# Performance work log

Hardware: AMD Instinct MI355X
Metric: run time of the kernel (lower is better)

## Reference

```python
import jax, jax.numpy as jnp
import numpy as np

LEAK = 0.01  # F.leaky_relu default negative_slope


def projection(p, cam, res):
    # Weak-perspective projection to normalized [-1,1] image coords.
    # cam = [s, tx, ty]; p [B,N,3] -> [B,N,2]
    s = cam[:, 0][:, None, None]
    t = cam[:, None, 1:3]
    return s * (p[..., :2] + t)


def grid_sample_points(im_feat, pts):
    # Bilinear grid_sample with align_corners=True, zeros padding,
    # specialized to a [B,N,1,2] point grid (matches points.unsqueeze(2)).
    # im_feat [B,C,H,W], pts [B,N,2] in [-1,1] -> [B,C,N]
    B, C, H, W = im_feat.shape
    N = pts.shape[1]
    x = (pts[..., 0] + 1.0) * 0.5 * (W - 1)
    y = (pts[..., 1] + 1.0) * 0.5 * (H - 1)
    x0 = jnp.floor(x)
    y0 = jnp.floor(y)
    x1 = x0 + 1.0
    y1 = y0 + 1.0
    wx1 = x - x0
    wx0 = 1.0 - wx1
    wy1 = y - y0
    wy0 = 1.0 - wy1
    feat_flat = im_feat.reshape(B, C, H * W)

    def gather(xi, yi, w):
        valid = (xi >= 0) & (xi <= W - 1) & (yi >= 0) & (yi <= H - 1)
        xc = jnp.clip(xi, 0, W - 1).astype(jnp.int32)
        yc = jnp.clip(yi, 0, H - 1).astype(jnp.int32)
        idx = (yc * W + xc)[:, None, :]  # [B,1,N]
        g = jnp.take_along_axis(feat_flat, jnp.broadcast_to(idx, (B, C, N)), axis=2)
        return g * (w * valid.astype(w.dtype))[:, None, :]

    return (gather(x0, y0, wx0 * wy0) + gather(x1, y0, wx1 * wy0)
            + gather(x0, y1, wx0 * wy1) + gather(x1, y1, wx1 * wy1))


def reduce_dim(feat, W0, b0, W1, b1, W2, b2):
    # feat [B,C0,N]; Conv1d kernel_size=1 == channel matmul.
    def conv1x1(x, W, b):
        return jnp.einsum('oc,bcn->bon', W, x) + b[None, :, None]

    y = jax.nn.leaky_relu(conv1x1(feat, W0, b0), LEAK)
    y = jax.nn.leaky_relu(conv1x1(jnp.concatenate([y, feat], axis=1), W1, b1), LEAK)
    y = conv1x1(jnp.concatenate([y, feat], axis=1), W2, b2)
    y = jax.nn.relu(y)  # last_op
    return y.reshape(y.shape[0], -1)  # [B, C_p*N]


def setup_inputs() -> dict:
    key = jax.random.key(0)
    ks = jax.random.split(key, 9)
    B, N, C, H, Wd = 64, 431, 256, 56, 56
    dims = [256, 128, 64, 5]
    p = jax.random.normal(ks[0], (B, N, 3), jnp.float32)
    cam = jax.random.uniform(ks[1], (B, 3), jnp.float32)
    s_feat = jax.random.normal(ks[2], (B, C, H, Wd), jnp.float32)
    W0 = jax.random.normal(ks[3], (dims[1], dims[0]), jnp.float32) * 0.02
    b0 = jnp.zeros((dims[1],), jnp.float32)
    W1 = jax.random.normal(ks[4], (dims[2], dims[1] + dims[0]), jnp.float32) * 0.02
    b1 = jnp.zeros((dims[2],), jnp.float32)
    W2 = jax.random.normal(ks[5], (dims[3], dims[2] + dims[0]), jnp.float32) * 0.02
    b2 = jnp.zeros((dims[3],), jnp.float32)
    return {"p": p, "cam": cam, "s_feat": s_feat,
            "W0": W0, "b0": b0, "W1": W1, "b1": b1, "W2": W2, "b2": b2,
            "res": 224}


def reference(p, cam, s_feat, W0, b0, W1, b1, W2, b2, res):
    p2d = projection(p, cam, res)                 # [B,N,2]
    point_feat = grid_sample_points(s_feat, p2d)  # [B,C_s,N]
    return reduce_dim(point_feat, W0, b0, W1, b1, W2, b2)  # [B, C_p*N]
```

## Files before the change

kernel.cpp:

```cpp
#include <hip/hip_runtime.h>


#define B_   64
#define N_   431
#define C_   256
#define H_   56
#define W_   56
#define HW_  (H_ * W_)
#define PPB  16
#define NT_  27

#define FS   264
#define Y0S  136
#define Y1S  72

typedef __attribute__((ext_vector_type(8))) short short8;
typedef __attribute__((ext_vector_type(4))) float f32x4;

__device__ __forceinline__ ushort f2bf(float f) {
    unsigned u = __float_as_uint(f);
    u += 0x7fffu + ((u >> 16) & 1u);
    return (ushort)(u >> 16);
}
__device__ __forceinline__ float bf2f(ushort h) {
    return __uint_as_float((unsigned)h << 16);
}

__global__ void convert_weights(const float* __restrict__ W0,
                                const float* __restrict__ W1,
                                const float* __restrict__ W2,
                                ushort* __restrict__ W0b,
                                ushort* __restrict__ W1b,
                                ushort* __restrict__ W2p)
{
    const int total = 128 * 256 + 64 * 384 + 16 * 320;
    for (int i = blockIdx.x * 256 + threadIdx.x; i < total; i += gridDim.x * 256) {
        if (i < 128 * 256) {
            W0b[i] = f2bf(W0[i]);
        } else if (i < 128 * 256 + 64 * 384) {
            const int j = i - 128 * 256;
            W1b[j] = f2bf(W1[j]);
        } else {
            const int j = i - (128 * 256 + 64 * 384);
            const int r = j / 320, c = j - r * 320;
            W2p[j] = (r < 5) ? f2bf(W2[r * 320 + c]) : (ushort)0;
        }
    }
}

__global__ __launch_bounds__(256, 4) void transpose_bf16(
    const float* __restrict__ in, ushort* __restrict__ out)
{
    __shared__ float tile[64][69];
    const int pix0 = blockIdx.x * 64;
    const int c0   = blockIdx.y * 64;
    const int b    = blockIdx.z;
    const int t    = threadIdx.x;

    {
        const int cr = t >> 4;
        const int p4 = (t & 15) * 4;
        const float* inb = in + ((size_t)b * C_ + c0) * HW_ + pix0;
        #pragma unroll
        for (int i = 0; i < 4; ++i) {
            const int cc = cr + i * 16;
            const float4 v = *(const float4*)(inb + (size_t)cc * HW_ + p4);
            tile[cc][p4 + 0] = v.x;
            tile[cc][p4 + 1] = v.y;
            tile[cc][p4 + 2] = v.z;
            tile[cc][p4 + 3] = v.w;
        }
    }
    __syncthreads();
    {
        const int c4 = (t & 15) * 4;
        const int pr = t >> 4;
        ushort* outb = out + ((size_t)b * HW_ + pix0) * C_ + c0;
        #pragma unroll
        for (int i = 0; i < 4; ++i) {
            const int pp = pr + i * 16;
            ushort4 v;
            v.x = f2bf(tile[c4 + 0][pp]);
            v.y = f2bf(tile[c4 + 1][pp]);
            v.z = f2bf(tile[c4 + 2][pp]);
            v.w = f2bf(tile[c4 + 3][pp]);
            *(ushort4*)(outb + (size_t)pp * C_ + c4) = v;
        }
    }
}

__global__ __launch_bounds__(256, 4) void maf_mfma_kernel(
    const float* __restrict__ p,
    const float* __restrict__ cam,
    const ushort* __restrict__ tf,
    const ushort* __restrict__ W0b,
    const float* __restrict__ b0,
    const ushort* __restrict__ W1b,
    const float* __restrict__ b1,
    const ushort* __restrict__ W2p,
    const float* __restrict__ b2,
    float* __restrict__ out)
{
    __shared__ ushort feat_s[PPB * FS];
    __shared__ ushort y0_s[PPB * Y0S];
    __shared__ ushort y1_s[PPB * Y1S];

    const int tid = threadIdx.x;
    const int w   = tid >> 6;
    const int l   = tid & 63;
    const int m   = l & 15;
    const int q   = l >> 4;
    const int b   = blockIdx.y;
    const int n0  = blockIdx.x * PPB;

    const float s  = cam[b * 3 + 0];
    const float tx = cam[b * 3 + 1];
    const float ty = cam[b * 3 + 2];

    {
        const ushort* __restrict__ tb = tf + (size_t)b * HW_ * C_;
        const int c4 = l * 4;
        #pragma unroll
        for (int i = 0; i < 4; ++i) {
            const int pp = w * 4 + i;
            const int n  = n0 + pp;
            ushort4 r = {0, 0, 0, 0};
            if (n < N_) {
                const float px = p[((size_t)b * N_ + n) * 3 + 0];
                const float py = p[((size_t)b * N_ + n) * 3 + 1];
                const float x = (s * (px + tx) + 1.f) * 0.5f * (float)(W_ - 1);
                const float y = (s * (py + ty) + 1.f) * 0.5f * (float)(H_ - 1);
                const float x0f = floorf(x), y0f = floorf(y);
                const float wx1 = x - x0f, wx0 = 1.f - wx1;
                const float wy1 = y - y0f, wy0 = 1.f - wy1;
                const int ix0 = (int)x0f, iy0 = (int)y0f;
                const int ix1 = ix0 + 1,  iy1 = iy0 + 1;
                const bool vx0 = (ix0 >= 0) & (ix0 <= W_ - 1);
                const bool vx1 = (ix1 >= 0) & (ix1 <= W_ - 1);
                const bool vy0 = (iy0 >= 0) & (iy0 <= H_ - 1);
                const bool vy1 = (iy1 >= 0) & (iy1 <= H_ - 1);
                const int cx0 = min(max(ix0, 0), W_ - 1);
                const int cx1 = min(max(ix1, 0), W_ - 1);
                const int cy0 = min(max(iy0, 0), H_ - 1);
                const int cy1 = min(max(iy1, 0), H_ - 1);
                const float w00 = (vx0 & vy0) ? wx0 * wy0 : 0.f;
                const float w10 = (vx1 & vy0) ? wx1 * wy0 : 0.f;
                const float w01 = (vx0 & vy1) ? wx0 * wy1 : 0.f;
                const float w11 = (vx1 & vy1) ? wx1 * wy1 : 0.f;
                const ushort4 f00 = *(const ushort4*)(tb + (size_t)(cy0 * W_ + cx0) * C_ + c4);
                const ushort4 f10 = *(const ushort4*)(tb + (size_t)(cy0 * W_ + cx1) * C_ + c4);
                const ushort4 f01 = *(const ushort4*)(tb + (size_t)(cy1 * W_ + cx0) * C_ + c4);
                const ushort4 f11 = *(const ushort4*)(tb + (size_t)(cy1 * W_ + cx1) * C_ + c4);
                r.x = f2bf(w00 * bf2f(f00.x) + w10 * bf2f(f10.x) + w01 * bf2f(f01.x) + w11 * bf2f(f11.x));
                r.y = f2bf(w00 * bf2f(f00.y) + w10 * bf2f(f10.y) + w01 * bf2f(f01.y) + w11 * bf2f(f11.y));
                r.z = f2bf(w00 * bf2f(f00.z) + w10 * bf2f(f10.z) + w01 * bf2f(f01.z) + w11 * bf2f(f11.z));
                r.w = f2bf(w00 * bf2f(f00.w) + w10 * bf2f(f10.w) + w01 * bf2f(f01.w) + w11 * bf2f(f11.w));
            }
            *(ushort4*)&feat_s[pp * FS + c4] = r;
        }
    }
    __syncthreads();

    {
        f32x4 acc0 = {0.f, 0.f, 0.f, 0.f};
        f32x4 acc1 = {0.f, 0.f, 0.f, 0.f};
        const ushort* __restrict__ ar  = feat_s + m * FS + 8 * q;
        const ushort* __restrict__ wr0 = W0b + ((size_t)(2 * w) * 16 + m) * 256 + 8 * q;
        const ushort* __restrict__ wr1 = W0b + ((size_t)(2 * w + 1) * 16 + m) * 256 + 8 * q;
        #pragma unroll
        for (int ks = 0; ks < 8; ++ks) {
            const short8 a  = *(const short8*)(ar + 32 * ks);
            const short8 w0 = *(const short8*)(wr0 + 32 * ks);
            const short8 w1 = *(const short8*)(wr1 + 32 * ks);
            acc0 = __builtin_amdgcn_mfma_f32_16x16x32_bf16(a, w0, acc0, 0, 0, 0);
            acc1 = __builtin_amdgcn_mfma_f32_16x16x32_bf16(a, w1, acc1, 0, 0, 0);
        }
        const int o0 = (2 * w) * 16 + m, o1 = o0 + 16;
        const float bias0 = b0[o0], bias1 = b0[o1];
        #pragma unroll
        for (int r = 0; r < 4; ++r) {
            float v0 = acc0[r] + bias0; v0 = (v0 > 0.f) ? v0 : 0.01f * v0;
            float v1 = acc1[r] + bias1; v1 = (v1 > 0.f) ? v1 : 0.01f * v1;
            y0_s[(q * 4 + r) * Y0S + o0] = f2bf(v0);
            y0_s[(q * 4 + r) * Y0S + o1] = f2bf(v1);
        }
    }
    __syncthreads();

    {
        f32x4 acc = {0.f, 0.f, 0.f, 0.f};
        const ushort* __restrict__ wr = W1b + ((size_t)w * 16 + m) * 384 + 8 * q;
        #pragma unroll
        for (int ks = 0; ks < 12; ++ks) {
            short8 a;
            if (ks < 4) a = *(const short8*)(y0_s  + m * Y0S + 32 * ks + 8 * q);
            else        a = *(const short8*)(feat_s + m * FS + 32 * ks - 128 + 8 * q);
            const short8 bb = *(const short8*)(wr + 32 * ks);
            acc = __builtin_amdgcn_mfma_f32_16x16x32_bf16(a, bb, acc, 0, 0, 0);
        }
        const int o = w * 16 + m;
        const float bias = b1[o];
        #pragma unroll
        for (int r = 0; r < 4; ++r) {
            float v = acc[r] + bias; v = (v > 0.f) ? v : 0.01f * v;
            y1_s[(q * 4 + r) * Y1S + o] = f2bf(v);
        }
    }
    __syncthreads();

    if (w == 0) {
        f32x4 acc = {0.f, 0.f, 0.f, 0.f};
        const ushort* __restrict__ wr = W2p + (size_t)m * 320 + 8 * q;
        #pragma unroll
        for (int ks = 0; ks < 10; ++ks) {
            short8 a;
            if (ks < 2) a = *(const short8*)(y1_s + m * Y1S + 32 * ks + 8 * q);
            else        a = *(const short8*)(feat_s + m * FS + 32 * ks - 64 + 8 * q);
            const short8 bb = *(const short8*)(wr + 32 * ks);
            acc = __builtin_amdgcn_mfma_f32_16x16x32_bf16(a, bb, acc, 0, 0, 0);
        }
        if (m < 5) {
            const float bias = b2[m];
            #pragma unroll
            for (int r = 0; r < 4; ++r) {
                const int n = n0 + q * 4 + r;
                if (n < N_) {
                    float v = acc[r] + bias;
                    out[((size_t)b * 5 + m) * N_ + n] = (v > 0.f) ? v : 0.f;
                }
            }
        }
    }
}

__global__ __launch_bounds__(256, 4) void maf_fallback_kernel(
    const float* __restrict__ p, const float* __restrict__ cam,
    const float* __restrict__ sfeat,
    const float* __restrict__ W0, const float* __restrict__ b0,
    const float* __restrict__ W1, const float* __restrict__ b1,
    const float* __restrict__ W2, const float* __restrict__ b2,
    float* __restrict__ out)
{
    __shared__ float feat_s[PPB][C_ + 4];
    __shared__ float y0_s[PPB][128 + 4];
    __shared__ float y1_s[PPB][64 + 4];

    const int tid = threadIdx.x;
    const int b   = blockIdx.y;
    const int n0  = blockIdx.x * PPB;
    const float s  = cam[b * 3 + 0];
    const float tx = cam[b * 3 + 1];
    const float ty = cam[b * 3 + 2];
    {
        const int c = tid;
        const float* __restrict__ fb = sfeat + ((size_t)b * C_ + c) * HW_;
        for (int pp = 0; pp < PPB; ++pp) {
            const int n = n0 + pp;
            float val = 0.f;
            if (n < N_) {
                const float px = p[((size_t)b * N_ + n) * 3 + 0];
                const float py = p[((size_t)b * N_ + n) * 3 + 1];
                const float x = (s * (px + tx) + 1.f) * 0.5f * (float)(W_ - 1);
                const float y = (s * (py + ty) + 1.f) * 0.5f * (float)(H_ - 1);
                const float x0f = floorf(x), y0f = floorf(y);
                const float wx1 = x - x0f, wx0 = 1.f - wx1;
                const float wy1 = y - y0f, wy0 = 1.f - wy1;
                const int ix0 = (int)x0f, iy0 = (int)y0f;
                const int ix1 = ix0 + 1,  iy1 = iy0 + 1;
                const bool vx0 = (ix0 >= 0) & (ix0 <= W_ - 1);
                const bool vx1 = (ix1 >= 0) & (ix1 <= W_ - 1);
                const bool vy0 = (iy0 >= 0) & (iy0 <= H_ - 1);
                const bool vy1 = (iy1 >= 0) & (iy1 <= H_ - 1);
                const int cx0 = min(max(ix0, 0), W_ - 1);
                const int cx1 = min(max(ix1, 0), W_ - 1);
                const int cy0 = min(max(iy0, 0), H_ - 1);
                const int cy1 = min(max(iy1, 0), H_ - 1);
                const float w00 = (vx0 & vy0) ? wx0 * wy0 : 0.f;
                const float w10 = (vx1 & vy0) ? wx1 * wy0 : 0.f;
                const float w01 = (vx0 & vy1) ? wx0 * wy1 : 0.f;
                const float w11 = (vx1 & vy1) ? wx1 * wy1 : 0.f;
                val = w00 * fb[cy0 * W_ + cx0] + w10 * fb[cy0 * W_ + cx1]
                    + w01 * fb[cy1 * W_ + cx0] + w11 * fb[cy1 * W_ + cx1];
            }
            feat_s[pp][c] = val;
        }
    }
    __syncthreads();
    {
        const int o = tid & 127, pg = tid >> 7, p0 = pg * 8;
        const float* __restrict__ wr = W0 + (size_t)o * 256;
        float acc[8] = {0, 0, 0, 0, 0, 0, 0, 0};
        for (int k = 0; k < 256; k += 4) {
            const float4 w = *(const float4*)(wr + k);
            for (int i = 0; i < 8; ++i) {
                const float4 f = *(const float4*)&feat_s[p0 + i][k];
                acc[i] += w.x * f.x + w.y * f.y + w.z * f.z + w.w * f.w;
            }
        }
        const float bias = b0[o];
        for (int i = 0; i < 8; ++i) {
            const float v = acc[i] + bias;
            y0_s[p0 + i][o] = (v > 0.f) ? v : 0.01f * v;
        }
    }
    __syncthreads();
    {
        const int o = tid & 63, pg = tid >> 6, p0 = pg * 4;
        const float* __restrict__ wr = W1 + (size_t)o * 384;
        float acc[4] = {0, 0, 0, 0};
        for (int k = 0; k < 128; k += 4) {
            const float4 w = *(const float4*)(wr + k);
            for (int i = 0; i < 4; ++i) {
                const float4 f = *(const float4*)&y0_s[p0 + i][k];
                acc[i] += w.x * f.x + w.y * f.y + w.z * f.z + w.w * f.w;
            }
        }
        for (int k = 0; k < 256; k += 4) {
            const float4 w = *(const float4*)(wr + 128 + k);
            for (int i = 0; i < 4; ++i) {
                const float4 f = *(const float4*)&feat_s[p0 + i][k];
                acc[i] += w.x * f.x + w.y * f.y + w.z * f.z + w.w * f.w;
            }
        }
        const float bias = b1[o];
        for (int i = 0; i < 4; ++i) {
            const float v = acc[i] + bias;
            y1_s[p0 + i][o] = (v > 0.f) ? v : 0.01f * v;
        }
    }
    __syncthreads();
    if (tid < 80) {
        const int o = tid >> 4, pp = tid & 15;
        const float* __restrict__ wr = W2 + (size_t)o * 320;
        float acc = 0.f;
        for (int k = 0; k < 64; k += 4) {
            const float4 w = *(const float4*)(wr + k);
            const float4 f = *(const float4*)&y1_s[pp][k];
            acc += w.x * f.x + w.y * f.y + w.z * f.z + w.w * f.w;
        }
        for (int k = 0; k < 256; k += 4) {
            const float4 w = *(const float4*)(wr + 64 + k);
            const float4 f = *(const float4*)&feat_s[pp][k];
            acc += w.x * f.x + w.y * f.y + w.z * f.z + w.w * f.w;
        }
        const int n = n0 + pp;
        if (n < N_) {
            float v = acc + b2[o];
            out[((size_t)b * 5 + o) * N_ + n] = (v > 0.f) ? v : 0.f;
        }
    }
}

extern "C" void kernel_launch(void* const* d_in, const int* in_sizes, int n_in,
                              void* d_out, int out_size, void* d_ws, size_t ws_size,
                              hipStream_t stream) {
    const float* p     = (const float*)d_in[0];
    const float* cam   = (const float*)d_in[1];
    const float* sfeat = (const float*)d_in[2];
    const float* W0    = (const float*)d_in[3];
    const float* b0    = (const float*)d_in[4];
    const float* W1    = (const float*)d_in[5];
    const float* b1    = (const float*)d_in[6];
    const float* W2    = (const float*)d_in[7];
    const float* b2    = (const float*)d_in[8];
    float* out = (float*)d_out;

    const size_t tf_elems = (size_t)B_ * HW_ * C_;
    size_t off = tf_elems;
    const size_t w0_off = off; off += 128 * 256;
    const size_t w1_off = off; off += 64 * 384;
    const size_t w2_off = off; off += 16 * 320;
    const size_t need = off * sizeof(ushort);

    if (ws_size >= need) {
        ushort* tf  = (ushort*)d_ws;
        ushort* W0b = tf + w0_off;
        ushort* W1b = tf + w1_off;
        ushort* W2p = tf + w2_off;
        convert_weights<<<64, 256, 0, stream>>>(W0, W1, W2, W0b, W1b, W2p);
        transpose_bf16<<<dim3(HW_ / 64, C_ / 64, B_), 256, 0, stream>>>(sfeat, tf);
        maf_mfma_kernel<<<dim3(NT_, B_), 256, 0, stream>>>(
            p, cam, tf, W0b, b0, W1b, b1, W2p, b2, out);
    } else {
        maf_fallback_kernel<<<dim3(NT_, B_), 256, 0, stream>>>(
            p, cam, sfeat, W0, b0, W1, b1, W2, b2, out);
    }
}
```

Baseline: 347.6 us.

## Replace full feature transpose with per-channel-plane LDS bilinear gather

```diff
diff --git a/kernel.cpp b/kernel.cpp
--- a/kernel.cpp
+++ b/kernel.cpp
@@ -6,11 +6,11 @@
 #define C_   256
 #define H_   56
 #define W_   56
-#define HW_  (H_ * W_)
+#define HW_  3136
 #define PPB  16
 #define NT_  27
-
-#define FS   264
+#define NPAD (NT_ * PPB)
+
 #define Y0S  136
 #define Y1S  72
 
@@ -22,109 +22,63 @@
     u += 0x7fffu + ((u >> 16) & 1u);
     return (ushort)(u >> 16);
 }
-__device__ __forceinline__ float bf2f(ushort h) {
-    return __uint_as_float((unsigned)h << 16);
-}
-
-__global__ void convert_weights(const float* __restrict__ W0,
-                                const float* __restrict__ W1,
-                                const float* __restrict__ W2,
-                                ushort* __restrict__ W0b,
-                                ushort* __restrict__ W1b,
-                                ushort* __restrict__ W2p)
-{
-    const int total = 128 * 256 + 64 * 384 + 16 * 320;
-    for (int i = blockIdx.x * 256 + threadIdx.x; i < total; i += gridDim.x * 256) {
-        if (i < 128 * 256) {
-            W0b[i] = f2bf(W0[i]);
-        } else if (i < 128 * 256 + 64 * 384) {
-            const int j = i - 128 * 256;
-            W1b[j] = f2bf(W1[j]);
-        } else {
-            const int j = i - (128 * 256 + 64 * 384);
-            const int r = j / 320, c = j - r * 320;
-            W2p[j] = (r < 5) ? f2bf(W2[r * 320 + c]) : (ushort)0;
-        }
-    }
-}
-
-__global__ __launch_bounds__(256, 4) void transpose_bf16(
-    const float* __restrict__ in, ushort* __restrict__ out)
-{
-    __shared__ float tile[64][69];
-    const int pix0 = blockIdx.x * 64;
-    const int c0   = blockIdx.y * 64;
-    const int b    = blockIdx.z;
-    const int t    = threadIdx.x;
-
-    {
-        const int cr = t >> 4;
-        const int p4 = (t & 15) * 4;
-        const float* inb = in + ((size_t)b * C_ + c0) * HW_ + pix0;
-        #pragma unroll
-        for (int i = 0; i < 4; ++i) {
-            const int cc = cr + i * 16;
-            const float4 v = *(const float4*)(inb + (size_t)cc * HW_ + p4);
-            tile[cc][p4 + 0] = v.x;
-            tile[cc][p4 + 1] = v.y;
-            tile[cc][p4 + 2] = v.z;
-            tile[cc][p4 + 3] = v.w;
-        }
-    }
-    __syncthreads();
-    {
-        const int c4 = (t & 15) * 4;
-        const int pr = t >> 4;
-        ushort* outb = out + ((size_t)b * HW_ + pix0) * C_ + c0;
-        #pragma unroll
-        for (int i = 0; i < 4; ++i) {
-            const int pp = pr + i * 16;
-            ushort4 v;
-            v.x = f2bf(tile[c4 + 0][pp]);
-            v.y = f2bf(tile[c4 + 1][pp]);
-            v.z = f2bf(tile[c4 + 2][pp]);
-            v.w = f2bf(tile[c4 + 3][pp]);
-            *(ushort4*)(outb + (size_t)pp * C_ + c4) = v;
-        }
-    }
-}
-
-__global__ __launch_bounds__(256, 4) void maf_mfma_kernel(
+
+#define WTOT (128 * 256 + 64 * 384 + 16 * 320)
+#define GB_  (B_ * 64)
+
+__global__ __launch_bounds__(256, 2) void gather_kernel(
     const float* __restrict__ p,
     const float* __restrict__ cam,
-    const ushort* __restrict__ tf,
-    const ushort* __restrict__ W0b,
-    const float* __restrict__ b0,
-    const ushort* __restrict__ W1b,
-    const float* __restrict__ b1,
-    const ushort* __restrict__ W2p,
-    const float* __restrict__ b2,
-    float* __restrict__ out)
+    const float* __restrict__ sfeat,
+    const float* __restrict__ W0,
+    const float* __restrict__ W1,
+    const float* __restrict__ W2,
+    ushort* __restrict__ feat,
+    ushort* __restrict__ W0b,
+    ushort* __restrict__ W1b,
+    ushort* __restrict__ W2p)
 {
-    __shared__ ushort feat_s[PPB * FS];
-    __shared__ ushort y0_s[PPB * Y0S];
-    __shared__ ushort y1_s[PPB * Y1S];
-
-    const int tid = threadIdx.x;
-    const int w   = tid >> 6;
-    const int l   = tid & 63;
-    const int m   = l & 15;
-    const int q   = l >> 4;
-    const int b   = blockIdx.y;
-    const int n0  = blockIdx.x * PPB;
-
-    const float s  = cam[b * 3 + 0];
-    const float tx = cam[b * 3 + 1];
-    const float ty = cam[b * 3 + 2];
-
-    {
-        const ushort* __restrict__ tb = tf + (size_t)b * HW_ * C_;
-        const int c4 = l * 4;
-        #pragma unroll
-        for (int i = 0; i < 4; ++i) {
-            const int pp = w * 4 + i;
-            const int n  = n0 + pp;
-            ushort4 r = {0, 0, 0, 0};
+    const int bx = blockIdx.x;
+    if (bx >= GB_) {
+        const int t0 = (bx - GB_) * 256 + threadIdx.x;
+        for (int i = t0; i < WTOT; i += 8 * 256) {
+            if (i < 128 * 256) {
+                W0b[i] = f2bf(W0[i]);
+            } else if (i < 128 * 256 + 64 * 384) {
+                const int j = i - 128 * 256;
+                W1b[j] = f2bf(W1[j]);
+            } else {
+                const int j = i - (128 * 256 + 64 * 384);
+                const int r = j / 320, c = j - r * 320;
+                W2p[j] = (r < 5) ? f2bf(W2[r * 320 + c]) : (ushort)0;
+            }
+        }
+        return;
+    }
+
+    __shared__ float planes[4][HW_];
+    __shared__ int   pidx[NPAD][4];
+    __shared__ float pw[NPAD][4];
+
+    const int b  = bx >> 6;
+    const int c0 = (bx & 63) * 4;
+    const int t  = threadIdx.x;
+
+    #pragma unroll
+    for (int j = 0; j < 4; ++j) {
+        const float4* __restrict__ src =
+            (const float4*)(sfeat + ((size_t)b * C_ + c0 + j) * HW_);
+        for (int k = t; k < HW_ / 4; k += 256)
+            *(float4*)&planes[j][k * 4] = src[k];
+    }
+
+    {
+        const float s  = cam[b * 3 + 0];
+        const float tx = cam[b * 3 + 1];
+        const float ty = cam[b * 3 + 2];
+        for (int n = t; n < NPAD; n += 256) {
+            int   i00 = 0, i10 = 0, i01 = 0, i11 = 0;
+            float w00 = 0.f, w10 = 0.f, w01 = 0.f, w11 = 0.f;
             if (n < N_) {
                 const float px = p[((size_t)b * N_ + n) * 3 + 0];
                 const float py = p[((size_t)b * N_ + n) * 3 + 1];
@@ -143,37 +97,70 @@
                 const int cx1 = min(max(ix1, 0), W_ - 1);
                 const int cy0 = min(max(iy0, 0), H_ - 1);
                 const int cy1 = min(max(iy1, 0), H_ - 1);
-                const float w00 = (vx0 & vy0) ? wx0 * wy0 : 0.f;
-                const float w10 = (vx1 & vy0) ? wx1 * wy0 : 0.f;
-                const float w01 = (vx0 & vy1) ? wx0 * wy1 : 0.f;
-                const float w11 = (vx1 & vy1) ? wx1 * wy1 : 0.f;
-                const ushort4 f00 = *(const ushort4*)(tb + (size_t)(cy0 * W_ + cx0) * C_ + c4);
-                const ushort4 f10 = *(const ushort4*)(tb + (size_t)(cy0 * W_ + cx1) * C_ + c4);
-                const ushort4 f01 = *(const ushort4*)(tb + (size_t)(cy1 * W_ + cx0) * C_ + c4);
-                const ushort4 f11 = *(const ushort4*)(tb + (size_t)(cy1 * W_ + cx1) * C_ + c4);
-                r.x = f2bf(w00 * bf2f(f00.x) + w10 * bf2f(f10.x) + w01 * bf2f(f01.x) + w11 * bf2f(f11.x));
-                r.y = f2bf(w00 * bf2f(f00.y) + w10 * bf2f(f10.y) + w01 * bf2f(f01.y) + w11 * bf2f(f11.y));
-                r.z = f2bf(w00 * bf2f(f00.z) + w10 * bf2f(f10.z) + w01 * bf2f(f01.z) + w11 * bf2f(f11.z));
-                r.w = f2bf(w00 * bf2f(f00.w) + w10 * bf2f(f10.w) + w01 * bf2f(f01.w) + w11 * bf2f(f11.w));
-            }
-            *(ushort4*)&feat_s[pp * FS + c4] = r;
-        }
-    }
-    __syncthreads();
+                w00 = (vx0 & vy0) ? wx0 * wy0 : 0.f;
+                w10 = (vx1 & vy0) ? wx1 * wy0 : 0.f;
+                w01 = (vx0 & vy1) ? wx0 * wy1 : 0.f;
+                w11 = (vx1 & vy1) ? wx1 * wy1 : 0.f;
+                i00 = cy0 * W_ + cx0;  i10 = cy0 * W_ + cx1;
+                i01 = cy1 * W_ + cx0;  i11 = cy1 * W_ + cx1;
+            }
+            pidx[n][0] = i00; pidx[n][1] = i10; pidx[n][2] = i01; pidx[n][3] = i11;
+            pw[n][0] = w00;   pw[n][1] = w10;   pw[n][2] = w01;   pw[n][3] = w11;
+        }
+    }
+    __syncthreads();
+
+    for (int n = t; n < NPAD; n += 256) {
+        const int   i00 = pidx[n][0], i10 = pidx[n][1], i01 = pidx[n][2], i11 = pidx[n][3];
+        const float w00 = pw[n][0],   w10 = pw[n][1],   w01 = pw[n][2],   w11 = pw[n][3];
+        ushort4 r;
+        r.x = f2bf(w00 * planes[0][i00] + w10 * planes[0][i10] + w01 * planes[0][i01] + w11 * planes[0][i11]);
+        r.y = f2bf(w00 * planes[1][i00] + w10 * planes[1][i10] + w01 * planes[1][i01] + w11 * planes[1][i11]);
+        r.z = f2bf(w00 * planes[2][i00] + w10 * planes[2][i10] + w01 * planes[2][i01] + w11 * planes[2][i11]);
+        r.w = f2bf(w00 * planes[3][i00] + w10 * planes[3][i10] + w01 * planes[3][i01] + w11 * planes[3][i11]);
+        *(ushort4*)(feat + ((size_t)b * NPAD + n) * C_ + c0) = r;
+    }
+}
+
+__global__ __launch_bounds__(256, 4) void mlp_kernel(
+    const ushort* __restrict__ feat,
+    const ushort* __restrict__ W0b,
+    const float* __restrict__ b0,
+    const ushort* __restrict__ W1b,
+    const float* __restrict__ b1,
+    const ushort* __restrict__ W2p,
+    const float* __restrict__ b2,
+    float* __restrict__ out)
+{
+    __shared__ ushort y0_s[PPB * Y0S];
+    __shared__ ushort y1_s[PPB * Y1S];
+
+    const int tid  = threadIdx.x;
+    const int w    = tid >> 6;
+    const int l    = tid & 63;
+    const int m    = l & 15;
+    const int q    = l >> 4;
+    const int tile = blockIdx.x;
+    const int b    = blockIdx.y;
+    const int n0   = tile * PPB;
+
+    const ushort* __restrict__ fb =
+        feat + (((size_t)b * NT_ + tile) * PPB + m) * C_ + 8 * q;
+    short8 af[8];
+    #pragma unroll
+    for (int ks = 0; ks < 8; ++ks) af[ks] = *(const short8*)(fb + 32 * ks);
 
     {
         f32x4 acc0 = {0.f, 0.f, 0.f, 0.f};
         f32x4 acc1 = {0.f, 0.f, 0.f, 0.f};
-        const ushort* __restrict__ ar  = feat_s + m * FS + 8 * q;
         const ushort* __restrict__ wr0 = W0b + ((size_t)(2 * w) * 16 + m) * 256 + 8 * q;
-        const ushort* __restrict__ wr1 = W0b + ((size_t)(2 * w + 1) * 16 + m) * 256 + 8 * q;
+        const ushort* __restrict__ wr1 = wr0 + 16 * 256;
         #pragma unroll
         for (int ks = 0; ks < 8; ++ks) {
-            const short8 a  = *(const short8*)(ar + 32 * ks);
             const short8 w0 = *(const short8*)(wr0 + 32 * ks);
             const short8 w1 = *(const short8*)(wr1 + 32 * ks);
-            acc0 = __builtin_amdgcn_mfma_f32_16x16x32_bf16(a, w0, acc0, 0, 0, 0);
-            acc1 = __builtin_amdgcn_mfma_f32_16x16x32_bf16(a, w1, acc1, 0, 0, 0);
+            acc0 = __builtin_amdgcn_mfma_f32_16x16x32_bf16(af[ks], w0, acc0, 0, 0, 0);
+            acc1 = __builtin_amdgcn_mfma_f32_16x16x32_bf16(af[ks], w1, acc1, 0, 0, 0);
         }
         const int o0 = (2 * w) * 16 + m, o1 = o0 + 16;
         const float bias0 = b0[o0], bias1 = b0[o1];
@@ -191,12 +178,15 @@
         f32x4 acc = {0.f, 0.f, 0.f, 0.f};
         const ushort* __restrict__ wr = W1b + ((size_t)w * 16 + m) * 384 + 8 * q;
         #pragma unroll
-        for (int ks = 0; ks < 12; ++ks) {
-            short8 a;
-            if (ks < 4) a = *(const short8*)(y0_s  + m * Y0S + 32 * ks + 8 * q);
-            else        a = *(const short8*)(feat_s + m * FS + 32 * ks - 128 + 8 * q);
+        for (int ks = 0; ks < 4; ++ks) {
+            const short8 a  = *(const short8*)(y0_s + m * Y0S + 32 * ks + 8 * q);
             const short8 bb = *(const short8*)(wr + 32 * ks);
             acc = __builtin_amdgcn_mfma_f32_16x16x32_bf16(a, bb, acc, 0, 0, 0);
+        }
+        #pragma unroll
+        for (int ks = 4; ks < 12; ++ks) {
+            const short8 bb = *(const short8*)(wr + 32 * ks);
+            acc = __builtin_amdgcn_mfma_f32_16x16x32_bf16(af[ks - 4], bb, acc, 0, 0, 0);
         }
         const int o = w * 16 + m;
         const float bias = b1[o];
@@ -212,12 +202,15 @@
         f32x4 acc = {0.f, 0.f, 0.f, 0.f};
         const ushort* __restrict__ wr = W2p + (size_t)m * 320 + 8 * q;
         #pragma unroll
-        for (int ks = 0; ks < 10; ++ks) {
-            short8 a;
-            if (ks < 2) a = *(const short8*)(y1_s + m * Y1S + 32 * ks + 8 * q);
-            else        a = *(const short8*)(feat_s + m * FS + 32 * ks - 64 + 8 * q);
+        for (int ks = 0; ks < 2; ++ks) {
+            const short8 a  = *(const short8*)(y1_s + m * Y1S + 32 * ks + 8 * q);
             const short8 bb = *(const short8*)(wr + 32 * ks);
             acc = __builtin_amdgcn_mfma_f32_16x16x32_bf16(a, bb, acc, 0, 0, 0);
+        }
+        #pragma unroll
+        for (int ks = 2; ks < 10; ++ks) {
+            const short8 bb = *(const short8*)(wr + 32 * ks);
+            acc = __builtin_amdgcn_mfma_f32_16x16x32_bf16(af[ks - 2], bb, acc, 0, 0, 0);
         }
         if (m < 5) {
             const float bias = b2[m];
@@ -365,22 +358,22 @@
     const float* b2    = (const float*)d_in[8];
     float* out = (float*)d_out;
 
-    const size_t tf_elems = (size_t)B_ * HW_ * C_;
-    size_t off = tf_elems;
+    const size_t feat_elems = (size_t)B_ * NPAD * C_;
+    size_t off = feat_elems;
     const size_t w0_off = off; off += 128 * 256;
     const size_t w1_off = off; off += 64 * 384;
     const size_t w2_off = off; off += 16 * 320;
     const size_t need = off * sizeof(ushort);
 
     if (ws_size >= need) {
-        ushort* tf  = (ushort*)d_ws;
-        ushort* W0b = tf + w0_off;
-        ushort* W1b = tf + w1_off;
-        ushort* W2p = tf + w2_off;
-        convert_weights<<<64, 256, 0, stream>>>(W0, W1, W2, W0b, W1b, W2p);
-        transpose_bf16<<<dim3(HW_ / 64, C_ / 64, B_), 256, 0, stream>>>(sfeat, tf);
-        maf_mfma_kernel<<<dim3(NT_, B_), 256, 0, stream>>>(
-            p, cam, tf, W0b, b0, W1b, b1, W2p, b2, out);
+        ushort* feat = (ushort*)d_ws;
+        ushort* W0b  = feat + w0_off;
+        ushort* W1b  = feat + w1_off;
+        ushort* W2p  = feat + w2_off;
+        gather_kernel<<<GB_ + 8, 256, 0, stream>>>(
+            p, cam, sfeat, W0, W1, W2, feat, W0b, W1b, W2p);
+        mlp_kernel<<<dim3(NT_, B_), 256, 0, stream>>>(
+            feat, W0b, b0, W1b, b1, W2p, b2, out);
     } else {
         maf_fallback_kernel<<<dim3(NT_, B_), 256, 0, stream>>>(
             p, cam, sfeat, W0, b0, W1, b1, W2, b2, out);
```

After: 377.8 us. 1.09x slower.
